# Optimization experiments

Hardware: AMD Instinct MI355X
Metric: run time of the kernel (lower is better)

## Reference

```python
import jax, jax.numpy as jnp
import numpy as np
import math

NUM_HEADS = 16
N_WIRES = 8  # == d_k


def setup_inputs() -> dict:
    key = jax.random.key(0)
    k1, k2, k3, k4 = jax.random.split(key, 4)
    B, S, E = 4, 2048, NUM_HEADS * N_WIRES
    x = jax.random.normal(k1, (B, S, E), dtype=jnp.float32)
    theta = jax.random.normal(k2, (N_WIRES,), dtype=jnp.float32)
    W_combine = jax.random.normal(k3, (E, E), dtype=jnp.float32) * (1.0 / math.sqrt(E))
    b_combine = jax.random.normal(k4, (E,), dtype=jnp.float32) * 0.01
    return {"x": x, "theta": theta, "W_combine": W_combine, "b_combine": b_combine}


def _quantum_heads(x, theta, H, dk):
    # since single-qubit RX gates compose and the state stays a product state.
    B, S, E = x.shape
    proj = x.reshape(B, S, H, dk)  # [B,S,H,dk]
    return jnp.cos(proj + theta)   # theta broadcasts over wires (dk == n_wires)


def reference(x, theta, W_combine, b_combine):
    B, S, E = x.shape
    H, dk = NUM_HEADS, N_WIRES
    qkv = _quantum_heads(x, theta, H, dk)          # [B,S,H,dk]; q = k = v
    qh = jnp.transpose(qkv, (0, 2, 1, 3))           # [B,H,S,dk]
    scores = jnp.einsum('bhqd,bhkd->bhqk', qh, qh) / math.sqrt(dk)
    attn = jax.nn.softmax(scores, axis=-1)          # [B,H,S,S]
    out = jnp.einsum('bhqk,bhkd->bhqd', attn, qh)   # [B,H,S,dk]
    out = jnp.transpose(out, (0, 2, 1, 3)).reshape(B, S, E)
    return out @ W_combine.T + b_combine
```

## Files before the change

### kernel.cpp

```cpp
#include <hip/hip_runtime.h>

typedef _Float16 f16;
typedef _Float16 f16x2 __attribute__((ext_vector_type(2)));
typedef _Float16 f16x4 __attribute__((ext_vector_type(4)));
typedef float    f32x4 __attribute__((ext_vector_type(4)));
typedef unsigned int u32;
typedef unsigned int u32x2v __attribute__((ext_vector_type(2)));

#define NS 2048
#define NH 16
#define NDK 8
#define NE 128
#define CHUNK 512
#define NCHUNK 4
#define CSCALE 0.51006972f
#define ONE2 0x3C003C00u

__device__ __forceinline__ float fexp2(float v){
#if __has_builtin(__builtin_amdgcn_exp2f)
  return __builtin_amdgcn_exp2f(v);
#else
  return exp2f(v);
#endif
}

__device__ __forceinline__ f16x2 pkrtz(float a, float b){
  return __builtin_bit_cast(f16x2, __builtin_amdgcn_cvt_pkrtz(a, b));
}

__device__ __forceinline__ float fdot2a(f16x2 a, f16x2 b, float c){
#if __has_builtin(__builtin_amdgcn_fdot2)
  return __builtin_amdgcn_fdot2(a, b, c, false);
#else
  return c + (float)a[0]*(float)b[0] + (float)a[1]*(float)b[1];
#endif
}

#define GLOAD16(g, l) __builtin_amdgcn_global_load_lds( \
    (const __attribute__((address_space(1))) u32*)(g), \
    (__attribute__((address_space(3))) u32*)(l), 16, 0, 0)

__global__ __launch_bounds__(256) void qcos(const float* __restrict__ x,
                                            const float* __restrict__ theta,
                                            u32* __restrict__ kbuf,
                                            u32* __restrict__ vbuf){
  __shared__ __align__(16) uint4 Lt[16*17];
  const int bid = blockIdx.x;
  const int b   = bid >> 7;
  const int t   = bid & 127;
  const int tid = threadIdx.x;

  const float4 thA = ((const float4*)theta)[0];
  const float4 thB = ((const float4*)theta)[1];

  {
    const int sl = tid & 15, h = tid >> 4;
    const int s  = t*16 + sl;
    const float* xp = x + ((size_t)(b*NS + s)*NE + h*NDK);
    const float4 x0 = ((const float4*)xp)[0];
    const float4 x1 = ((const float4*)xp)[1];
    union { f16 hh[8]; uint4 u; } pk;
    pk.hh[0] = (f16)__cosf(x0.x + thA.x);
    pk.hh[1] = (f16)__cosf(x0.y + thA.y);
    pk.hh[2] = (f16)__cosf(x0.z + thA.z);
    pk.hh[3] = (f16)__cosf(x0.w + thA.w);
    pk.hh[4] = (f16)__cosf(x1.x + thB.x);
    pk.hh[5] = (f16)__cosf(x1.y + thB.y);
    pk.hh[6] = (f16)__cosf(x1.z + thB.z);
    pk.hh[7] = (f16)__cosf(x1.w + thB.w);
    ((uint4*)kbuf)[(size_t)(b*16 + h)*NS + s] = pk.u;
    Lt[h*17 + sl] = pk.u;
  }
  __syncthreads();

  {
    const int h  = tid >> 4;
    const int d  = (tid >> 1) & 7;
    const int gp = tid & 1;
    const unsigned short* Ls = (const unsigned short*)Lt;
    union { unsigned short us[8]; uint4 u; } pk;
    #pragma unroll
    for(int j = 0; j < 8; ++j)
      pk.us[j] = Ls[(h*17 + 8*gp + j)*8 + d];
    ((uint4*)vbuf)[((size_t)(b*16 + h)*128 + t)*16 + d*2 + gp] = pk.u;
  }
}

#define QTILE(T, VPO, KPO, ACCA, ACCB) do{ \
    uint2 ka_ = (KPO)[(T)*32]; \
    uint2 va_ = (VPO)[(T)*32]; \
    u32 w0_ = creal ? va_.x : ONE2; \
    u32 w1_ = creal ? va_.y : ONE2; \
    u32x2v vu_ = { w0_, w1_ }; \
    f16x4 kf_ = __builtin_bit_cast(f16x4, ka_); \
    f16x4 vf_ = __builtin_bit_cast(f16x4, vu_); \
    f32x4 s0_ = __builtin_amdgcn_mfma_f32_16x16x16f16(kf_, qf0, z4, 0, 0, 0); \
    f32x4 s1_ = __builtin_amdgcn_mfma_f32_16x16x16f16(kf_, qf1, z4, 0, 0, 0); \
    f16x2 a0_ = pkrtz(fexp2(s0_[0]), fexp2(s0_[1])); \
    f16x2 b0_ = pkrtz(fexp2(s0_[2]), fexp2(s0_[3])); \
    f16x2 a1_ = pkrtz(fexp2(s1_[0]), fexp2(s1_[1])); \
    f16x2 b1_ = pkrtz(fexp2(s1_[2]), fexp2(s1_[3])); \
    u32x2v p0_ = { __builtin_bit_cast(u32, a0_), __builtin_bit_cast(u32, b0_) }; \
    u32x2v p1_ = { __builtin_bit_cast(u32, a1_), __builtin_bit_cast(u32, b1_) }; \
    ACCA = __builtin_amdgcn_mfma_f32_16x16x16f16(vf_, __builtin_bit_cast(f16x4, p0_), ACCA, 0, 0, 0); \
    ACCB = __builtin_amdgcn_mfma_f32_16x16x16f16(vf_, __builtin_bit_cast(f16x4, p1_), ACCB, 0, 0, 0); \
  }while(0)

__global__ __launch_bounds__(512, 4) void qattn(const u32* __restrict__ kbuf,
                                                const u32* __restrict__ vbuf,
                                                float* __restrict__ out){
  __shared__ __align__(16) u32 Kc[2][2048];
  __shared__ __align__(16) u32 Vt[2][2048];

  const int bid  = blockIdx.x;
  const int bh   = bid >> 3;
  const int qc   = bid & 7;
  const int tid  = threadIdx.x;
  const int lane = tid & 63;
  const int w    = tid >> 6;
  const int c    = lane & 15;
  const int grp  = lane >> 4;
  const int g1   = grp & 1;
  const bool lo32  = lane < 32;
  const bool creal = c < 8;

  const u32* kb = kbuf + (size_t)bh*8192;
  const u32* vb = vbuf + (size_t)bh*8192;

  const u32* gk = kb + (size_t)tid*4;
  const u32* gv = vb + (size_t)tid*4;

  const int qrow0 = qc*256 + w*32 + c;
  const int qrow1 = qrow0 + 16;
  uint2 qv0 = make_uint2(0u, 0u), qv1 = make_uint2(0u, 0u);
  if(lo32){
    qv0 = *(const uint2*)(kb + (size_t)qrow0*4 + g1*2);
    qv1 = *(const uint2*)(kb + (size_t)qrow1*4 + g1*2);
  }
  f16x4 q40 = __builtin_bit_cast(f16x4, qv0);
  f16x4 q41 = __builtin_bit_cast(f16x4, qv1);
  q40 *= (f16)CSCALE;
  q41 *= (f16)CSCALE;
  const f16x4 qf0 = q40, qf1 = q41;

  const u32 vlane = ((u32)(c & 7))*32u + ((u32)grp)*8u;

  const f32x4 z4 = {0.f, 0.f, 0.f, 0.f};
  f32x4 accA0 = z4, accB0 = z4;
  f32x4 accA1 = z4, accB1 = z4;

  GLOAD16(gk, &Kc[0][w*256]);
  GLOAD16(gv, &Vt[0][w*256]);

  for(int cc = 0; cc < NCHUNK; ++cc){
    __syncthreads();
    if(cc + 1 < NCHUNK){
      GLOAD16(gk + (size_t)(cc+1)*2048, &Kc[(cc+1)&1][w*256]);
      GLOAD16(gv + (size_t)(cc+1)*2048, &Vt[(cc+1)&1][w*256]);
    }
    const uint2* kp = (const uint2*)&Kc[cc&1][0] + c*2 + g1;
    const uint2* vp = (const uint2*)((const char*)&Vt[cc&1][0] + vlane);
    #pragma unroll
    for(int o = 0; o < 4; ++o){
      const uint2* kpo = kp + o*256;
      const uint2* vpo = vp + o*256;
      QTILE(0, vpo, kpo, accA0, accA1);
      QTILE(1, vpo, kpo, accB0, accB1);
      QTILE(2, vpo, kpo, accA0, accA1);
      QTILE(3, vpo, kpo, accB0, accB1);
      QTILE(4, vpo, kpo, accA0, accA1);
      QTILE(5, vpo, kpo, accB0, accB1);
      QTILE(6, vpo, kpo, accA0, accA1);
      QTILE(7, vpo, kpo, accB0, accB1);
    }
  }

  const int b = bh >> 4, h = bh & 15;
  {
    f32x4 aT;
    aT[0]=accA0[0]+accB0[0]; aT[1]=accA0[1]+accB0[1];
    aT[2]=accA0[2]+accB0[2]; aT[3]=accA0[3]+accB0[3];
    float den = __shfl(aT[0], 32 + c, 64);
    if(lo32){
      float inv = 1.0f / den;
      float4 o;
      o.x = aT[0]*inv; o.y = aT[1]*inv; o.z = aT[2]*inv; o.w = aT[3]*inv;
      *(float4*)(out + ((size_t)(b*NS + qrow0)*NH + h)*NDK + grp*4) = o;
    }
  }
  {
    f32x4 aT;
    aT[0]=accA1[0]+accB1[0]; aT[1]=accA1[1]+accB1[1];
    aT[2]=accA1[2]+accB1[2]; aT[3]=accA1[3]+accB1[3];
    float den = __shfl(aT[0], 32 + c, 64);
    if(lo32){
      float inv = 1.0f / den;
      float4 o;
      o.x = aT[0]*inv; o.y = aT[1]*inv; o.z = aT[2]*inv; o.w = aT[3]*inv;
      *(float4*)(out + ((size_t)(b*NS + qrow1)*NH + h)*NDK + grp*4) = o;
    }
  }
}

__global__ __launch_bounds__(256) void qcomb(const float* __restrict__ W,
                                             const float* __restrict__ bias,
                                             float* __restrict__ io){
  __shared__ __align__(16) u32 Wt[64*132];
  __shared__ __align__(16) u32 A2[32*65];
  const int tid = threadIdx.x;
  const size_t row0 = (size_t)blockIdx.x * 32;

  #pragma unroll
  for(int i=0;i<32;++i){
    int g = tid + 256*i;
    int j = g >> 6, e2 = g & 63;
    const float* wp = W + (size_t)j*NE + 2*e2;
    f16x2 wv = pkrtz(wp[0], wp[1]);
    Wt[e2*132 + j] = __builtin_bit_cast(u32, wv);
  }
  #pragma unroll
  for(int i=0;i<8;++i){
    int g = tid + 256*i;
    int r = g >> 6, e2 = g & 63;
    const float* ap = io + (row0 + r)*NE + 2*e2;
    f16x2 av = pkrtz(ap[0], ap[1]);
    A2[r*65 + e2] = __builtin_bit_cast(u32, av);
  }
  __syncthreads();

  const int tr = tid >> 4, tc = tid & 15;
  float acc0[8] = {0,0,0,0,0,0,0,0};
  float acc1[8] = {0,0,0,0,0,0,0,0};
  for(int e2=0; e2<64; ++e2){
    f16x2 a0 = __builtin_bit_cast(f16x2, A2[tr*65 + e2]);
    f16x2 a1 = __builtin_bit_cast(f16x2, A2[(tr+16)*65 + e2]);
    const u32* wr = &Wt[e2*132 + tc*8];
    #pragma unroll
    for(int cj=0; cj<8; ++cj){
      f16x2 wv = __builtin_bit_cast(f16x2, wr[cj]);
      acc0[cj] = fdot2a(a0, wv, acc0[cj]);
      acc1[cj] = fdot2a(a1, wv, acc1[cj]);
    }
  }

  float4 b0 = *(const float4*)(bias + tc*8);
  float4 b1 = *(const float4*)(bias + tc*8 + 4);
  float* o0 = io + (row0 + tr)*NE + tc*8;
  float* o1 = io + (row0 + tr + 16)*NE + tc*8;
  float4 v;
  v.x = acc0[0]+b0.x; v.y = acc0[1]+b0.y; v.z = acc0[2]+b0.z; v.w = acc0[3]+b0.w;
  *(float4*)(o0) = v;
  v.x = acc0[4]+b1.x; v.y = acc0[5]+b1.y; v.z = acc0[6]+b1.z; v.w = acc0[7]+b1.w;
  *(float4*)(o0+4) = v;
  v.x = acc1[0]+b0.x; v.y = acc1[1]+b0.y; v.z = acc1[2]+b0.z; v.w = acc1[3]+b0.w;
  *(float4*)(o1) = v;
  v.x = acc1[4]+b1.x; v.y = acc1[5]+b1.y; v.z = acc1[6]+b1.z; v.w = acc1[7]+b1.w;
  *(float4*)(o1+4) = v;
}

extern "C" void kernel_launch(void* const* d_in, const int* in_sizes, int n_in,
                              void* d_out, int out_size, void* d_ws, size_t ws_size,
                              hipStream_t stream) {
  (void)in_sizes; (void)n_in; (void)out_size; (void)ws_size;
  const float* x     = (const float*)d_in[0];
  const float* theta = (const float*)d_in[1];
  const float* W     = (const float*)d_in[2];
  const float* bias  = (const float*)d_in[3];
  float* out = (float*)d_out;
  u32* kbuf = (u32*)d_ws;
  u32* vbuf = kbuf + 524288;

  qcos <<<512, 256, 0, stream>>>(x, theta, kbuf, vbuf);
  qattn<<<512, 512, 0, stream>>>(kbuf, vbuf, out);
  qcomb<<<256, 256, 0, stream>>>(W, bias, out);
}
```

Before: 51.05 us.

## Swizzle V layout, stagger per-wave tile order, and prefetch LDS operands one tile ahead

The V buffer layout is XOR-swizzled by d, and the LDS read offset is adjusted to match, to spread accesses across banks. Each wave now starts its inner sub-chunk loop at a different offset (w-rotated) to reduce LDS contention between waves. The K/V LDS loads for the next tile are issued before the current tile's MFMA/exp work, a software-pipelining step that hides LDS latency. This costs extra registers, which could affect occupancy at 512x4 launch bounds.

```diff
diff --git a/kernel.cpp b/kernel.cpp
--- a/kernel.cpp
+++ b/kernel.cpp
@@ -82,17 +82,16 @@
     #pragma unroll
     for(int j = 0; j < 8; ++j)
       pk.us[j] = Ls[(h*17 + 8*gp + j)*8 + d];
-    ((uint4*)vbuf)[((size_t)(b*16 + h)*128 + t)*16 + d*2 + gp] = pk.u;
-  }
-}
-
-#define QTILE(T, VPO, KPO, ACCA, ACCB) do{ \
-    uint2 ka_ = (KPO)[(T)*32]; \
-    uint2 va_ = (VPO)[(T)*32]; \
-    u32 w0_ = creal ? va_.x : ONE2; \
-    u32 w1_ = creal ? va_.y : ONE2; \
+    const int slot = d*2 + (gp ^ ((d >> 2) & 1));
+    ((uint4*)vbuf)[((size_t)(b*16 + h)*128 + t)*16 + slot] = pk.u;
+  }
+}
+
+#define QCOMP(KA, VA, ACCA, ACCB) do{ \
+    u32 w0_ = creal ? (VA).x : ONE2; \
+    u32 w1_ = creal ? (VA).y : ONE2; \
     u32x2v vu_ = { w0_, w1_ }; \
-    f16x4 kf_ = __builtin_bit_cast(f16x4, ka_); \
+    f16x4 kf_ = __builtin_bit_cast(f16x4, (KA)); \
     f16x4 vf_ = __builtin_bit_cast(f16x4, vu_); \
     f32x4 s0_ = __builtin_amdgcn_mfma_f32_16x16x16f16(kf_, qf0, z4, 0, 0, 0); \
     f32x4 s1_ = __builtin_amdgcn_mfma_f32_16x16x16f16(kf_, qf1, z4, 0, 0, 0); \
@@ -106,6 +105,13 @@
     ACCB = __builtin_amdgcn_mfma_f32_16x16x16f16(vf_, __builtin_bit_cast(f16x4, p1_), ACCB, 0, 0, 0); \
   }while(0)
 
+#define QSTEP(TN, ACCA, ACCB) do{ \
+    uint2 kn_ = kpo[(TN)*32]; \
+    uint2 vn_ = vpo[(TN)*32]; \
+    QCOMP(ka, va, ACCA, ACCB); \
+    ka = kn_; va = vn_; \
+  }while(0)
+
 __global__ __launch_bounds__(512, 4) void qattn(const u32* __restrict__ kbuf,
                                                 const u32* __restrict__ vbuf,
                                                 float* __restrict__ out){
@@ -143,7 +149,9 @@
   q41 *= (f16)CSCALE;
   const f16x4 qf0 = q40, qf1 = q41;
 
-  const u32 vlane = ((u32)(c & 7))*32u + ((u32)grp)*8u;
+  const u32 vlane = ((u32)(c & 7))*32u
+                  + (u32)((((grp >> 1) ^ ((c >> 2) & 1)))*16)
+                  + ((u32)(grp & 1))*8u;
 
   const f32x4 z4 = {0.f, 0.f, 0.f, 0.f};
   f32x4 accA0 = z4, accB0 = z4;
@@ -161,17 +169,19 @@
     const uint2* kp = (const uint2*)&Kc[cc&1][0] + c*2 + g1;
     const uint2* vp = (const uint2*)((const char*)&Vt[cc&1][0] + vlane);
     #pragma unroll
-    for(int o = 0; o < 4; ++o){
+    for(int oo = 0; oo < 4; ++oo){
+      const int o = (oo + w) & 3;
       const uint2* kpo = kp + o*256;
       const uint2* vpo = vp + o*256;
-      QTILE(0, vpo, kpo, accA0, accA1);
-      QTILE(1, vpo, kpo, accB0, accB1);
-      QTILE(2, vpo, kpo, accA0, accA1);
-      QTILE(3, vpo, kpo, accB0, accB1);
-      QTILE(4, vpo, kpo, accA0, accA1);
-      QTILE(5, vpo, kpo, accB0, accB1);
-      QTILE(6, vpo, kpo, accA0, accA1);
-      QTILE(7, vpo, kpo, accB0, accB1);
+      uint2 ka = kpo[0], va = vpo[0];
+      QSTEP(1, accA0, accA1);
+      QSTEP(2, accB0, accB1);
+      QSTEP(3, accA0, accA1);
+      QSTEP(4, accB0, accB1);
+      QSTEP(5, accA0, accA1);
+      QSTEP(6, accB0, accB1);
+      QSTEP(7, accA0, accA1);
+      QCOMP(ka, va, accB0, accB1);
     }
   }
 
```

New measurement: 50.86 us. Within noise of the previous version (-0.4%).

## Stream K/V directly from global into registers instead of LDS staging

Applied to the files above, without the earlier changes.

The attention kernel stops staging K and V chunks through double-buffered LDS with async global-to-LDS loads and barriers. Each wave now reads its K/V tiles straight from global/L2 into registers, with a software prefetch one group of eight tiles ahead. The grid is also reshaped to 1024 blocks of 256 threads, each covering 128 query rows. This removes the LDS traffic and __syncthreads, but every wave now re-reads the same K/V from cache and register pressure goes up.

```diff
diff --git a/kernel.cpp b/kernel.cpp
--- a/kernel.cpp
+++ b/kernel.cpp
@@ -11,8 +11,6 @@
 #define NH 16
 #define NDK 8
 #define NE 128
-#define CHUNK 512
-#define NCHUNK 4
 #define CSCALE 0.51006972f
 #define ONE2 0x3C003C00u
 
@@ -35,10 +33,6 @@
   return c + (float)a[0]*(float)b[0] + (float)a[1]*(float)b[1];
 #endif
 }
-
-#define GLOAD16(g, l) __builtin_amdgcn_global_load_lds( \
-    (const __attribute__((address_space(1))) u32*)(g), \
-    (__attribute__((address_space(3))) u32*)(l), 16, 0, 0)
 
 __global__ __launch_bounds__(256) void qcos(const float* __restrict__ x,
                                             const float* __restrict__ theta,
@@ -86,13 +80,11 @@
   }
 }
 
-#define QTILE(T, VPO, KPO, ACCA, ACCB) do{ \
-    uint2 ka_ = (KPO)[(T)*32]; \
-    uint2 va_ = (VPO)[(T)*32]; \
-    u32 w0_ = creal ? va_.x : ONE2; \
-    u32 w1_ = creal ? va_.y : ONE2; \
+#define QCOMP(KA, VA, ACCA, ACCB) do{ \
+    u32 w0_ = creal ? (VA).x : ONE2; \
+    u32 w1_ = creal ? (VA).y : ONE2; \
     u32x2v vu_ = { w0_, w1_ }; \
-    f16x4 kf_ = __builtin_bit_cast(f16x4, ka_); \
+    f16x4 kf_ = __builtin_bit_cast(f16x4, (KA)); \
     f16x4 vf_ = __builtin_bit_cast(f16x4, vu_); \
     f32x4 s0_ = __builtin_amdgcn_mfma_f32_16x16x16f16(kf_, qf0, z4, 0, 0, 0); \
     f32x4 s1_ = __builtin_amdgcn_mfma_f32_16x16x16f16(kf_, qf1, z4, 0, 0, 0); \
@@ -106,15 +98,12 @@
     ACCB = __builtin_amdgcn_mfma_f32_16x16x16f16(vf_, __builtin_bit_cast(f16x4, p1_), ACCB, 0, 0, 0); \
   }while(0)
 
-__global__ __launch_bounds__(512, 4) void qattn(const u32* __restrict__ kbuf,
+__global__ __launch_bounds__(256, 4) void qattn(const u32* __restrict__ kbuf,
                                                 const u32* __restrict__ vbuf,
                                                 float* __restrict__ out){
-  __shared__ __align__(16) u32 Kc[2][2048];
-  __shared__ __align__(16) u32 Vt[2][2048];
-
   const int bid  = blockIdx.x;
-  const int bh   = bid >> 3;
-  const int qc   = bid & 7;
+  const int bh   = bid >> 4;
+  const int qc   = bid & 15;
   const int tid  = threadIdx.x;
   const int lane = tid & 63;
   const int w    = tid >> 6;
@@ -127,10 +116,7 @@
   const u32* kb = kbuf + (size_t)bh*8192;
   const u32* vb = vbuf + (size_t)bh*8192;
 
-  const u32* gk = kb + (size_t)tid*4;
-  const u32* gv = vb + (size_t)tid*4;
-
-  const int qrow0 = qc*256 + w*32 + c;
+  const int qrow0 = qc*128 + w*32 + c;
   const int qrow1 = qrow0 + 16;
   uint2 qv0 = make_uint2(0u, 0u), qv1 = make_uint2(0u, 0u);
   if(lo32){
@@ -143,37 +129,40 @@
   q41 *= (f16)CSCALE;
   const f16x4 qf0 = q40, qf1 = q41;
 
-  const u32 vlane = ((u32)(c & 7))*32u + ((u32)grp)*8u;
+  const uint2* kp = (const uint2*)kb + (c*2 + g1);
+  const uint2* vp = (const uint2*)vb + ((c & 7)*4 + grp);
 
   const f32x4 z4 = {0.f, 0.f, 0.f, 0.f};
   f32x4 accA0 = z4, accB0 = z4;
   f32x4 accA1 = z4, accB1 = z4;
 
-  GLOAD16(gk, &Kc[0][w*256]);
-  GLOAD16(gv, &Vt[0][w*256]);
-
-  for(int cc = 0; cc < NCHUNK; ++cc){
-    __syncthreads();
-    if(cc + 1 < NCHUNK){
-      GLOAD16(gk + (size_t)(cc+1)*2048, &Kc[(cc+1)&1][w*256]);
-      GLOAD16(gv + (size_t)(cc+1)*2048, &Vt[(cc+1)&1][w*256]);
-    }
-    const uint2* kp = (const uint2*)&Kc[cc&1][0] + c*2 + g1;
-    const uint2* vp = (const uint2*)((const char*)&Vt[cc&1][0] + vlane);
-    #pragma unroll
-    for(int o = 0; o < 4; ++o){
-      const uint2* kpo = kp + o*256;
-      const uint2* vpo = vp + o*256;
-      QTILE(0, vpo, kpo, accA0, accA1);
-      QTILE(1, vpo, kpo, accB0, accB1);
-      QTILE(2, vpo, kpo, accA0, accA1);
-      QTILE(3, vpo, kpo, accB0, accB1);
-      QTILE(4, vpo, kpo, accA0, accA1);
-      QTILE(5, vpo, kpo, accB0, accB1);
-      QTILE(6, vpo, kpo, accA0, accA1);
-      QTILE(7, vpo, kpo, accB0, accB1);
-    }
-  }
+  uint2 kr0,kr1,kr2,kr3,kr4,kr5,kr6,kr7;
+  uint2 vr0,vr1,vr2,vr3,vr4,vr5,vr6,vr7;
+  kr0=kp[0*32]; vr0=vp[0*32];  kr1=kp[1*32]; vr1=vp[1*32];
+  kr2=kp[2*32]; vr2=vp[2*32];  kr3=kp[3*32]; vr3=vp[3*32];
+  kr4=kp[4*32]; vr4=vp[4*32];  kr5=kp[5*32]; vr5=vp[5*32];
+  kr6=kp[6*32]; vr6=vp[6*32];  kr7=kp[7*32]; vr7=vp[7*32];
+
+  for(int t = 0; t < 120; t += 8){
+    const uint2* kn = kp + (t+8)*32;
+    const uint2* vn = vp + (t+8)*32;
+    { uint2 ka=kr0, va=vr0; kr0=kn[0*32]; vr0=vn[0*32]; QCOMP(ka, va, accA0, accA1); }
+    { uint2 ka=kr1, va=vr1; kr1=kn[1*32]; vr1=vn[1*32]; QCOMP(ka, va, accB0, accB1); }
+    { uint2 ka=kr2, va=vr2; kr2=kn[2*32]; vr2=vn[2*32]; QCOMP(ka, va, accA0, accA1); }
+    { uint2 ka=kr3, va=vr3; kr3=kn[3*32]; vr3=vn[3*32]; QCOMP(ka, va, accB0, accB1); }
+    { uint2 ka=kr4, va=vr4; kr4=kn[4*32]; vr4=vn[4*32]; QCOMP(ka, va, accA0, accA1); }
+    { uint2 ka=kr5, va=vr5; kr5=kn[5*32]; vr5=vn[5*32]; QCOMP(ka, va, accB0, accB1); }
+    { uint2 ka=kr6, va=vr6; kr6=kn[6*32]; vr6=vn[6*32]; QCOMP(ka, va, accA0, accA1); }
+    { uint2 ka=kr7, va=vr7; kr7=kn[7*32]; vr7=vn[7*32]; QCOMP(ka, va, accB0, accB1); }
+  }
+  QCOMP(kr0, vr0, accA0, accA1);
+  QCOMP(kr1, vr1, accB0, accB1);
+  QCOMP(kr2, vr2, accA0, accA1);
+  QCOMP(kr3, vr3, accB0, accB1);
+  QCOMP(kr4, vr4, accA0, accA1);
+  QCOMP(kr5, vr5, accB0, accB1);
+  QCOMP(kr6, vr6, accA0, accA1);
+  QCOMP(kr7, vr7, accB0, accB1);
 
   const int b = bh >> 4, h = bh & 15;
   {
@@ -271,6 +260,6 @@
   u32* vbuf = kbuf + 524288;
 
   qcos <<<512, 256, 0, stream>>>(x, theta, kbuf, vbuf);
-  qattn<<<512, 512, 0, stream>>>(kbuf, vbuf, out);
+  qattn<<<1024, 256, 0, stream>>>(kbuf, vbuf, out);
   qcomb<<<256, 256, 0, stream>>>(W, bias, out);
 }
```

Measured after the change: 53.98 us. 5.7% more time.
